# Kernel tuning notes

Measured on AMD Instinct MI355X. Metric: run time of the kernel, lower is better.

Reference implementation:

```python
import jax, jax.numpy as jnp
import numpy as np

B, N, C_IN, C_OUT = 2, 512, 64, 64  # mid_dim == out_dim
EPS = 1e-5

def _bn(x, g, b):
    # PyTorch BatchNorm1d in training mode: biased batch stats over axis 0 of [M, C]
    mu = x.mean(axis=0)
    var = x.var(axis=0)
    return (x - mu) * jax.lax.rsqrt(var + EPS) * g + b

def setup_inputs() -> dict:
    key = jax.random.key(0)
    ks = jax.random.split(key, 16)
    s = 0.05
    return {
        "pos": jax.random.normal(ks[0], (B, N, 3), jnp.float32),
        "c_features": jax.random.normal(ks[1], (B, N, C_IN), jnp.float32),
        "Wq": jax.random.normal(ks[2], (C_OUT, C_IN), jnp.float32) * s,
        "bq": jnp.zeros((C_OUT,), jnp.float32),
        "Wk": jax.random.normal(ks[3], (C_OUT, C_IN), jnp.float32) * s,
        "bk": jnp.zeros((C_OUT,), jnp.float32),
        "Wv": jax.random.normal(ks[4], (C_OUT, C_IN), jnp.float32) * s,
        "bv": jnp.zeros((C_OUT,), jnp.float32),
        "Wp1": jax.random.normal(ks[5], (3, 3), jnp.float32) * s,
        "bp1": jnp.zeros((3,), jnp.float32),
        "g_p": jnp.ones((3,), jnp.float32),
        "b_p": jnp.zeros((3,), jnp.float32),
        "Wp2": jax.random.normal(ks[6], (C_OUT, 3), jnp.float32) * s,
        "bp2": jnp.zeros((C_OUT,), jnp.float32),
        "g_w": jnp.ones((C_OUT,), jnp.float32),
        "b_w": jnp.zeros((C_OUT,), jnp.float32),
        "Ww1": jax.random.normal(ks[7], (C_OUT, C_OUT), jnp.float32) * s,
        "bw1": jnp.zeros((C_OUT,), jnp.float32),
        "Ww2": jax.random.normal(ks[8], (C_OUT, C_OUT), jnp.float32) * s,
        "bw2": jnp.zeros((C_OUT,), jnp.float32),
    }

def reference(pos, c_features, Wq, bq, Wk, bk, Wv, bv, Wp1, bp1, g_p, b_p, Wp2, bp2, g_w, b_w, Ww1, bw1, Ww2, bw2):
    b, n = pos.shape[0], pos.shape[1]
    q = c_features @ Wq.T + bq                       # [B,N,Cmid]
    k = c_features @ Wk.T + bk
    v = c_features @ Wv.T + bv                       # [B,N,Cout]
    rel = pos[:, :, None, :] - pos[:, None, :, :]    # [B,N,N,3]
    h = rel.reshape(-1, 3) @ Wp1.T + bp1             # [B*N*N,3]
    h = jax.nn.relu(_bn(h, g_p, b_p))
    delta = (h @ Wp2.T + bp2).reshape(b, n, n, -1)   # [B,N,N,Cmid]
    qk = q[:, :, None, :] - k[:, None, :, :] + delta # [B,N,N,Cmid]
    h2 = _bn(qk.reshape(-1, qk.shape[-1]), g_w, b_w)
    h2 = jax.nn.relu(h2)
    h2 = jax.nn.relu(h2 @ Ww1.T + bw1)
    w = (h2 @ Ww2.T + bw2).reshape(b, n, n, -1)      # [B,N,N,Cout]
    attn = jax.nn.softmax(w, axis=2)                 # softmax over j
    out = jnp.sum(attn * (v[:, None, :, :] + delta), axis=2)  # [B,N,Cout]
    return out
```

## Files before the change

kernel.cpp:

```cpp
#include <hip/hip_runtime.h>
#include <stdint.h>
#include <stddef.h>

#define DEV __device__ __forceinline__

typedef __attribute__((ext_vector_type(4))) float f32x4;
typedef __attribute__((ext_vector_type(8))) short bf16x8;

union FragU { bf16x8 f; uint32_t u[4]; };

DEV uint32_t pk_bf16(float a, float b) {
  uint32_t d;
  asm("v_cvt_pk_bf16_f32 %0, %1, %2" : "=v"(d) : "v"(a), "v"(b));
  return d;
}

DEV uint16_t f2bf(float x) {
  uint32_t u = __float_as_uint(x);
  u += 0x7fffu + ((u >> 16) & 1u);
  return (uint16_t)(u >> 16);
}

__launch_bounds__(256)
__global__ void kP(const float* __restrict__ cf, const float* __restrict__ pos,
                   const float* __restrict__ Wq, const float* __restrict__ Wk,
                   const float* __restrict__ Wv, const float* __restrict__ bq,
                   const float* __restrict__ bk, const float* __restrict__ bv,
                   const float* __restrict__ Ww1, const float* __restrict__ Ww2,
                   const float* __restrict__ Wp1, const float* __restrict__ g_p,
                   const float* __restrict__ bp2,
                   float* __restrict__ qo, float* __restrict__ ko,
                   float* __restrict__ vT, uint16_t* __restrict__ W1bf,
                   uint16_t* __restrict__ W2bf, float* __restrict__ a1out,
                   unsigned int* __restrict__ counter) {
  const int bid = blockIdx.x, t = threadIdx.x;
  if (bid < 256) {
    __shared__ float cfl[4][64];
    const int rr = t >> 6, c = t & 63;
    const int r0 = bid * 4;
    cfl[rr][c] = cf[(size_t)(r0 + rr) * 64 + c];
    __syncthreads();
    const int bn = r0 + rr;
    const float* wqr = Wq + c * 64;
    const float* wkr = Wk + c * 64;
    const float* wvr = Wv + c * 64;
    float aq = bq[c], ak = bk[c], av = bv[c] + bp2[c];
#pragma unroll 8
    for (int kk = 0; kk < 64; ++kk) {
      const float f = cfl[rr][kk];
      aq = fmaf(f, wqr[kk], aq);
      ak = fmaf(f, wkr[kk], ak);
      av = fmaf(f, wvr[kk], av);
    }
    qo[(size_t)bn * 64 + c] = aq;
    ko[(size_t)bn * 64 + c] = ak;
    vT[((size_t)(bn >> 9) * 64 + c) * 512 + (bn & 511)] = av;
  } else if (bid == 256) {
    for (int idx = t; idx < 8192; idx += 256) {
      const int m = idx >> 12;
      const int r = idx & 4095;
      const int f = r >> 9;
      const int l = (r >> 3) & 63;
      const int e = r & 7;
      const int nt = f >> 1, ks = f & 1, lm = l & 15, lq = l >> 4;
      const int row = 16 * nt + lm, col = 8 * lq + 32 * ks + e;
      const float src = m ? Ww2[row * 64 + col] : Ww1[row * 64 + col];
      (m ? W2bf : W1bf)[r] = f2bf(src);
    }
  } else {
    if (t == 0) counter[0] = 0u;
    __shared__ float acc9[2][9];
    __shared__ float red[256][10];
    __shared__ float red2[9][16];
    for (int b = 0; b < 2; ++b) {
      float s[9];
#pragma unroll
      for (int a = 0; a < 9; ++a) s[a] = 0.f;
      for (int r = 0; r < 2; ++r) {
        int i = t + 256 * r;
        const float* p = pos + (size_t)(b * 512 + i) * 3;
        float p0 = p[0], p1 = p[1], p2 = p[2];
        s[0] += p0; s[1] += p1; s[2] += p2;
        s[3] += p0 * p0; s[4] += p0 * p1; s[5] += p0 * p2;
        s[6] += p1 * p1; s[7] += p1 * p2; s[8] += p2 * p2;
      }
#pragma unroll
      for (int a = 0; a < 9; ++a) red[t][a] = s[a];
      __syncthreads();
      if (t < 144) {
        const int a = t >> 4, p = t & 15;
        float v = 0.f;
#pragma unroll
        for (int qq = 0; qq < 16; ++qq) v += red[p * 16 + qq][a];
        red2[a][p] = v;
      }
      __syncthreads();
      if (t < 9) {
        float v = 0.f;
#pragma unroll
        for (int p = 0; p < 16; ++p) v += red2[t][p];
        acc9[b][t] = v;
      }
      __syncthreads();
    }
    if (t == 0) {
      float C[6] = {0.f, 0.f, 0.f, 0.f, 0.f, 0.f};
      const float invM = 1.0f / 524288.0f;
      for (int b = 0; b < 2; ++b) {
        float S0 = acc9[b][0], S1 = acc9[b][1], S2 = acc9[b][2];
        float G00 = acc9[b][3], G01 = acc9[b][4], G02 = acc9[b][5];
        float G11 = acc9[b][6], G12 = acc9[b][7], G22 = acc9[b][8];
        C[0] += 1024.f * G00 - 2.f * S0 * S0;
        C[1] += 1024.f * G01 - 2.f * S0 * S1;
        C[2] += 1024.f * G02 - 2.f * S0 * S2;
        C[3] += 1024.f * G11 - 2.f * S1 * S1;
        C[4] += 1024.f * G12 - 2.f * S1 * S2;
        C[5] += 1024.f * G22 - 2.f * S2 * S2;
      }
      for (int a = 0; a < 6; ++a) C[a] *= invM;
      for (int tt = 0; tt < 3; ++tt) {
        float w0 = Wp1[tt * 3 + 0], w1 = Wp1[tt * 3 + 1], w2 = Wp1[tt * 3 + 2];
        float var = w0 * w0 * C[0] + w1 * w1 * C[3] + w2 * w2 * C[5]
                  + 2.f * (w0 * w1 * C[1] + w0 * w2 * C[2] + w1 * w2 * C[4]);
        a1out[tt] = g_p[tt] * rsqrtf(var + 1e-5f);
      }
      a1out[3] = 0.f;
    }
  }
}

__launch_bounds__(256)
__global__ void kB(const float* __restrict__ pos, const float* __restrict__ a1,
                   const float* __restrict__ Wp1, const float* __restrict__ b_p,
                   const float* __restrict__ q, const float* __restrict__ k,
                   const float* __restrict__ bp2,
                   const float* __restrict__ g_w, const float* __restrict__ b_w,
                   const float* __restrict__ Wp2,
                   float* __restrict__ hpa, float* __restrict__ Mpart,
                   float* __restrict__ XPp, float* __restrict__ SNp,
                   unsigned int* __restrict__ counter,
                   float* __restrict__ a2o, float* __restrict__ be2o,
                   float* __restrict__ PtT) {
  const int bid = blockIdx.x, t = threadIdx.x;
  const int s = bid >> 4, b = (bid >> 3) & 1, chunk = bid & 7;

  __shared__ __align__(16) f32x4 X[512];
  __shared__ float U[64][64];
  __shared__ float redr[64][4][4];
  __shared__ float mred[256][6];
  __shared__ float mred2[64][6];
  __shared__ float rfin[64][4];
  __shared__ float redn[256][2];
  __shared__ float MfS[6];
  __shared__ float ShfS[3];
  __shared__ unsigned int isLast;

  {
    const float a10 = a1[0], a11 = a1[1], a12 = a1[2];
    const float w00 = Wp1[0], w01 = Wp1[1], w02 = Wp1[2];
    const float w10 = Wp1[3], w11 = Wp1[4], w12 = Wp1[5];
    const float w20 = Wp1[6], w21 = Wp1[7], w22 = Wp1[8];
    for (int r = 0; r < 2; ++r) {
      const int row = t + 256 * r;
      const float* p = pos + (size_t)(b * 512 + row) * 3;
      const float p0 = p[0], p1 = p[1], p2 = p[2];
      f32x4 v;
      v.x = a10 * (w00 * p0 + w01 * p1 + w02 * p2);
      v.y = a11 * (w10 * p0 + w11 * p1 + w12 * p2);
      v.z = a12 * (w20 * p0 + w21 * p1 + w22 * p2);
      v.w = 0.f;
      if (s == 0 && chunk == 0)
        *(f32x4*)(hpa + (size_t)(b * 512 + row) * 4) = v;
      if (s) { v.x = -v.x; v.y = -v.y; v.z = -v.z; }
      X[row] = v;
    }
  }
  {
    const float* src = s ? k : q;
    const int r0g = b * 512 + chunk * 64;
#pragma unroll
    for (int e = 0; e < 16; ++e) {
      const int idx = e * 256 + t;
      const int row = idx >> 6, c = idx & 63;
      float v = src[(size_t)(r0g + row) * 64 + c];
      if (!s) v += bp2[c];
      U[row][c] = v;
    }
  }
  __syncthreads();

  {
    const int al = t >> 2, qr = t & 3;
    const int a = chunk * 64 + al;
    const f32x4 xa = X[a];
    const float base0 = xa.x + b_p[0], base1 = xa.y + b_p[1], base2 = xa.z + b_p[2];
    float r0 = 0, r1 = 0, r2 = 0;
    float m00 = 0, m01 = 0, m02 = 0, m11 = 0, m12 = 0, m22 = 0;
#pragma unroll 8
    for (int jj = qr * 128; jj < qr * 128 + 128; ++jj) {
      const f32x4 xj = X[jj];
      const float h0 = fmaxf(0.f, base0 - xj.x);
      const float h1 = fmaxf(0.f, base1 - xj.y);
      const float h2 = fmaxf(0.f, base2 - xj.z);
      r0 += h0; r1 += h1; r2 += h2;
      if (s == 0) {
        m00 = fmaf(h0, h0, m00); m01 = fmaf(h0, h1, m01); m02 = fmaf(h0, h2, m02);
        m11 = fmaf(h1, h1, m11); m12 = fmaf(h1, h2, m12); m22 = fmaf(h2, h2, m22);
      }
    }
    redr[al][qr][0] = r0; redr[al][qr][1] = r1; redr[al][qr][2] = r2; redr[al][qr][3] = 0.f;
    mred[t][0] = m00; mred[t][1] = m01; mred[t][2] = m02;
    mred[t][3] = m11; mred[t][4] = m12; mred[t][5] = m22;
  }
  __syncthreads();

  if (t < 64) {
    float sx = 0, sy = 0, sz = 0;
#pragma unroll
    for (int p = 0; p < 4; ++p) { sx += redr[t][p][0]; sy += redr[t][p][1]; sz += redr[t][p][2]; }
    rfin[t][0] = sx; rfin[t][1] = sy; rfin[t][2] = sz; rfin[t][3] = 0.f;
    if (s == 0) {
#pragma unroll
      for (int cc = 0; cc < 6; ++cc)
        mred2[t][cc] = mred[t][cc] + mred[t + 64][cc] + mred[t + 128][cc] + mred[t + 192][cc];
    }
  }
  __syncthreads();

  if (s == 0 && t < 6) {
    float m = 0.f;
    for (int p = 0; p < 64; ++p) m += mred2[p][t];
    Mpart[bid * 12 + t] = m;
  }
  if (s == 0 && t >= 64 && t < 67) {
    const int tt = t - 64;
    float v = 0.f;
#pragma unroll 8
    for (int a = 0; a < 64; ++a) v += rfin[a][tt];
    Mpart[bid * 12 + 6 + tt] = v;
  }
  if (t < 192) {
    const int c = t & 63, tt = t >> 6;
    float xp = 0.f;
#pragma unroll 8
    for (int a = 0; a < 64; ++a) xp = fmaf(U[a][c], rfin[a][tt], xp);
    if (s) xp = -xp;
    XPp[((size_t)bid * 3 + tt) * 64 + c] = xp;
  }
  {
    const int c = t & 63, g = t >> 6;
    float su = 0.f, su2 = 0.f;
#pragma unroll
    for (int r = 0; r < 16; ++r) {
      const float v = U[g * 16 + r][c];
      su += v;
      su2 = fmaf(v, v, su2);
    }
    redn[t][0] = su; redn[t][1] = su2;
  }
  __syncthreads();
  if (t < 64) {
    float a0 = 0.f, a1v = 0.f;
#pragma unroll
    for (int p = 0; p < 4; ++p) { a0 += redn[t + 64 * p][0]; a1v += redn[t + 64 * p][1]; }
    SNp[((size_t)bid * 2 + 0) * 64 + t] = a0;
    SNp[((size_t)bid * 2 + 1) * 64 + t] = a1v;
  }

  __syncthreads();
  if (t == 0) {
    __threadfence();
    const unsigned int old = atomicAdd(counter, 1u);
    isLast = (old == 31u) ? 1u : 0u;
  }
  __syncthreads();
  if (isLast) {
    __threadfence();
    if (t < 6) {
      float m = 0.f;
#pragma unroll
      for (int p = 0; p < 16; ++p) m += Mpart[p * 12 + t];
      MfS[t] = m;
    }
    if (t >= 6 && t < 9) {
      const int tt = t - 6;
      float v = 0.f;
#pragma unroll
      for (int p = 0; p < 16; ++p) v += Mpart[p * 12 + 6 + tt];
      ShfS[tt] = v;
    }
    __syncthreads();
    if (t < 64) {
      const int c = t;
      float Su[2], Su2[2], Sk[2], Sk2[2];
#pragma unroll
      for (int bb = 0; bb < 2; ++bb) {
        float a0 = 0.f, a1v = 0.f, a2v = 0.f, a3 = 0.f;
#pragma unroll
        for (int p = 0; p < 8; ++p) {
          const int blkU = bb * 8 + p;
          const int blkK = 16 + bb * 8 + p;
          a0 += SNp[((size_t)blkU * 2 + 0) * 64 + c];
          a1v += SNp[((size_t)blkU * 2 + 1) * 64 + c];
          a2v += SNp[((size_t)blkK * 2 + 0) * 64 + c];
          a3 += SNp[((size_t)blkK * 2 + 1) * 64 + c];
        }
        Su[bb] = a0; Su2[bb] = a1v; Sk[bb] = a2v; Sk2[bb] = a3;
      }
      float URd0 = 0.f, URd1 = 0.f, URd2 = 0.f;
#pragma unroll
      for (int blk = 0; blk < 32; ++blk) {
        URd0 += XPp[((size_t)blk * 3 + 0) * 64 + c];
        URd1 += XPp[((size_t)blk * 3 + 1) * 64 + c];
        URd2 += XPp[((size_t)blk * 3 + 2) * 64 + c];
      }
      const float P0t = Wp2[c * 3 + 0], P1t = Wp2[c * 3 + 1], P2t = Wp2[c * 3 + 2];
      const float Nf = 512.f, invM = 1.f / 524288.f;
      float S1 = 0.f, Q2 = 0.f;
#pragma unroll
      for (int bb = 0; bb < 2; ++bb) {
        S1 += Nf * (Su[bb] - Sk[bb]);
        Q2 += Nf * Su2[bb] - 2.f * Su[bb] * Sk[bb] + Nf * Sk2[bb];
      }
      const float Xc = P0t * URd0 + P1t * URd1 + P2t * URd2;
      S1 += P0t * ShfS[0] + P1t * ShfS[1] + P2t * ShfS[2];
      const float Hm = P0t * P0t * MfS[0] + 2.f * P0t * P1t * MfS[1] + 2.f * P0t * P2t * MfS[2]
                     + P1t * P1t * MfS[3] + 2.f * P1t * P2t * MfS[4] + P2t * P2t * MfS[5];
      const float E1 = S1 * invM;
      const float E2 = (Q2 + 2.f * Xc + Hm) * invM;
      const float var = E2 - E1 * E1;
      const float rstd = rsqrtf(var + 1e-5f);
      const float A2 = g_w[c] * rstd;
      a2o[c] = A2;
      be2o[c] = b_w[c] - E1 * A2;
      PtT[0 * 64 + c] = A2 * P0t;
      PtT[1 * 64 + c] = A2 * P1t;
      PtT[2 * 64 + c] = A2 * P2t;
    }
  }
}

__launch_bounds__(256)
__global__ void k3_main(const float* __restrict__ q, const float* __restrict__ kk_,
                        const float* __restrict__ vT, const float* __restrict__ hpa,
                        const float* __restrict__ a2g, const float* __restrict__ be2g,
                        const float* __restrict__ PtTg,
                        const uint16_t* __restrict__ W1bf, const uint16_t* __restrict__ W2bf,
                        const float* __restrict__ bp2, const float* __restrict__ Wp2,
                        const float* __restrict__ b_p, const float* __restrict__ bw1g,
                        const float* __restrict__ bw2g, float* __restrict__ out) {
  const int bid = blockIdx.x;
  const int b = bid >> 9, i = bid & 511;
  const int t = threadIdx.x;
  const int wid = t >> 6, l = t & 63;
  const int lm = l & 15, lq = l >> 4;

  __shared__ __align__(16) uint16_t W1l[4096];
  __shared__ __align__(16) uint16_t W2l[4096];
  __shared__ __align__(16) uint16_t H2[4][16][76];
  __shared__ __align__(16) float P0[64];
  __shared__ __align__(16) float a2s[64];
  __shared__ __align__(16) float Pts[3][64];
  __shared__ __align__(16) float comb[4][64][2];

  {
    *(bf16x8*)(&W1l[t * 16])     = *(const bf16x8*)(W1bf + t * 16);
    *(bf16x8*)(&W1l[t * 16 + 8]) = *(const bf16x8*)(W1bf + t * 16 + 8);
    *(bf16x8*)(&W2l[t * 16])     = *(const bf16x8*)(W2bf + t * 16);
    *(bf16x8*)(&W2l[t * 16 + 8]) = *(const bf16x8*)(W2bf + t * 16 + 8);
  }
  if (t < 64) {
    const float a2v = a2g[t];
    a2s[t] = a2v;
    P0[t] = fmaf(a2v, q[(size_t)(b * 512 + i) * 64 + t] + bp2[t], be2g[t]);
  } else {
    const int idx = t - 64;
    Pts[idx >> 6][idx & 63] = PtTg[idx];
  }

  const f32x4 hi = *(const f32x4*)(hpa + (size_t)(b * 512 + i) * 4);
  const float bb0 = b_p[0], bb1 = b_p[1], bb2 = b_p[2];
  const float LOG2E = 1.4426950408889634f;

  float bw1r[4], bw2l[4], wpa[4], wpb[4], wpc[4];
#pragma unroll
  for (int nt = 0; nt < 4; ++nt) {
    const int c = 16 * nt + lm;
    bw1r[nt] = bw1g[c];
    bw2l[nt] = bw2g[c] * LOG2E;
    wpa[nt] = Wp2[c * 3 + 0];
    wpb[nt] = Wp2[c * 3 + 1];
    wpc[nt] = Wp2[c * 3 + 2];
  }

  float l_[4] = {0.f, 0.f, 0.f, 0.f};
  float acc_[4] = {0.f, 0.f, 0.f, 0.f};

  __syncthreads();

  const float* kbase = kk_ + (size_t)(b * 512) * 64;
  const float* hbase = hpa + (size_t)(b * 512) * 4;
  const float* vTb = vT + (size_t)b * 64 * 512;

  for (int it = 0; it < 8; ++it) {
    const int jb = it * 64 + wid * 16;
    const int j = jb + lm;
    const int j2 = jb + 4 * lq;

    f32x4 kv[2][2];
#pragma unroll
    for (int ks = 0; ks < 2; ++ks) {
      kv[ks][0] = *(const f32x4*)(kbase + (size_t)j * 64 + 32 * ks + 8 * lq);
      kv[ks][1] = *(const f32x4*)(kbase + (size_t)j * 64 + 32 * ks + 8 * lq + 4);
    }
    const f32x4 hj = *(const f32x4*)(hbase + j * 4);
    f32x4 hjr[4];
#pragma unroll
    for (int r = 0; r < 4; ++r) hjr[r] = *(const f32x4*)(hbase + (j2 + r) * 4);
    f32x4 vv[4];
#pragma unroll
    for (int nt = 0; nt < 4; ++nt)
      vv[nt] = *(const f32x4*)(vTb + (size_t)(16 * nt + lm) * 512 + j2);

    const float h0 = fmaxf(0.f, hi.x - hj.x + bb0);
    const float h1 = fmaxf(0.f, hi.y - hj.y + bb1);
    const float h2v = fmaxf(0.f, hi.z - hj.z + bb2);

    FragU A1[2];
#pragma unroll
    for (int ks = 0; ks < 2; ++ks) {
      const int c0 = 32 * ks + 8 * lq;
      f32x4 pv[2], av[2], t0[2], t1[2], t2[2];
      pv[0] = *(const f32x4*)(P0 + c0);        pv[1] = *(const f32x4*)(P0 + c0 + 4);
      av[0] = *(const f32x4*)(a2s + c0);       av[1] = *(const f32x4*)(a2s + c0 + 4);
      t0[0] = *(const f32x4*)(&Pts[0][c0]);    t0[1] = *(const f32x4*)(&Pts[0][c0 + 4]);
      t1[0] = *(const f32x4*)(&Pts[1][c0]);    t1[1] = *(const f32x4*)(&Pts[1][c0 + 4]);
      t2[0] = *(const f32x4*)(&Pts[2][c0]);    t2[1] = *(const f32x4*)(&Pts[2][c0 + 4]);
      float x[8];
#pragma unroll
      for (int e = 0; e < 8; ++e) {
        const int hh = e >> 2, e4 = e & 3;
        float xv = pv[hh][e4] - av[hh][e4] * kv[ks][hh][e4];
        xv = fmaf(t0[hh][e4], h0, xv);
        xv = fmaf(t1[hh][e4], h1, xv);
        xv = fmaf(t2[hh][e4], h2v, xv);
        x[e] = fmaxf(0.f, xv);
      }
      A1[ks].u[0] = pk_bf16(x[0], x[1]);
      A1[ks].u[1] = pk_bf16(x[2], x[3]);
      A1[ks].u[2] = pk_bf16(x[4], x[5]);
      A1[ks].u[3] = pk_bf16(x[6], x[7]);
    }

    f32x4 d1[4];
#pragma unroll
    for (int nt = 0; nt < 4; ++nt) {
      FragU b0, b1;
      b0.f = *(const bf16x8*)(&W1l[((nt * 2 + 0) * 64 + l) * 8]);
      b1.f = *(const bf16x8*)(&W1l[((nt * 2 + 1) * 64 + l) * 8]);
      f32x4 z = {0.f, 0.f, 0.f, 0.f};
      z = __builtin_amdgcn_mfma_f32_16x16x32_bf16(A1[0].f, b0.f, z, 0, 0, 0);
      z = __builtin_amdgcn_mfma_f32_16x16x32_bf16(A1[1].f, b1.f, z, 0, 0, 0);
      d1[nt] = z;
    }

    uint16_t (*h2w)[76] = H2[wid];
#pragma unroll
    for (int nt = 0; nt < 4; ++nt) {
      const float e0 = fmaxf(0.f, d1[nt][0] + bw1r[nt]);
      const float e1 = fmaxf(0.f, d1[nt][1] + bw1r[nt]);
      const float e2 = fmaxf(0.f, d1[nt][2] + bw1r[nt]);
      const float e3 = fmaxf(0.f, d1[nt][3] + bw1r[nt]);
      const uint32_t u01 = pk_bf16(e0, e1);
      const uint32_t u23 = pk_bf16(e2, e3);
      const int col = 16 * nt + lm;
      h2w[4 * lq + 0][col] = (uint16_t)(u01 & 0xffffu);
      h2w[4 * lq + 1][col] = (uint16_t)(u01 >> 16);
      h2w[4 * lq + 2][col] = (uint16_t)(u23 & 0xffffu);
      h2w[4 * lq + 3][col] = (uint16_t)(u23 >> 16);
    }

    FragU A2[2];
    A2[0].f = *(const bf16x8*)(&h2w[lm][8 * lq]);
    A2[1].f = *(const bf16x8*)(&h2w[lm][32 + 8 * lq]);

    f32x4 d2[4];
#pragma unroll
    for (int nt = 0; nt < 4; ++nt) {
      FragU b0, b1;
      b0.f = *(const bf16x8*)(&W2l[((nt * 2 + 0) * 64 + l) * 8]);
      b1.f = *(const bf16x8*)(&W2l[((nt * 2 + 1) * 64 + l) * 8]);
      f32x4 z = {0.f, 0.f, 0.f, 0.f};
      z = __builtin_amdgcn_mfma_f32_16x16x32_bf16(A2[0].f, b0.f, z, 0, 0, 0);
      z = __builtin_amdgcn_mfma_f32_16x16x32_bf16(A2[1].f, b1.f, z, 0, 0, 0);
      d2[nt] = z;
    }

    float hr0[4], hr1[4], hr2[4];
#pragma unroll
    for (int r = 0; r < 4; ++r) {
      hr0[r] = fmaxf(0.f, hi.x - hjr[r].x + bb0);
      hr1[r] = fmaxf(0.f, hi.y - hjr[r].y + bb1);
      hr2[r] = fmaxf(0.f, hi.z - hjr[r].z + bb2);
    }

#pragma unroll
    for (int nt = 0; nt < 4; ++nt) {
      float p[4], val[4];
#pragma unroll
      for (int r = 0; r < 4; ++r) {
        p[r] = __builtin_amdgcn_exp2f(fmaf(d2[nt][r], LOG2E, bw2l[nt]));
        float v0 = vv[nt][r];
        v0 = fmaf(wpa[nt], hr0[r], v0);
        v0 = fmaf(wpb[nt], hr1[r], v0);
        v0 = fmaf(wpc[nt], hr2[r], v0);
        val[r] = v0;
      }
      l_[nt] += (p[0] + p[1]) + (p[2] + p[3]);
      float a = acc_[nt];
      a = fmaf(p[0], val[0], a);
      a = fmaf(p[1], val[1], a);
      a = fmaf(p[2], val[2], a);
      a = fmaf(p[3], val[3], a);
      acc_[nt] = a;
    }
  }

#pragma unroll
  for (int nt = 0; nt < 4; ++nt) {
    l_[nt] += __shfl_xor(l_[nt], 16);
    acc_[nt] += __shfl_xor(acc_[nt], 16);
    l_[nt] += __shfl_xor(l_[nt], 32);
    acc_[nt] += __shfl_xor(acc_[nt], 32);
  }
  if (lq == 0) {
#pragma unroll
    for (int nt = 0; nt < 4; ++nt) {
      comb[wid][16 * nt + lm][0] = l_[nt];
      comb[wid][16 * nt + lm][1] = acc_[nt];
    }
  }
  __syncthreads();
  if (t < 64) {
    float L = 0.f, A = 0.f;
#pragma unroll
    for (int w = 0; w < 4; ++w) {
      L += comb[w][t][0];
      A += comb[w][t][1];
    }
    out[(size_t)(b * 512 + i) * 64 + t] = A / L;
  }
}

extern "C" void kernel_launch(void* const* d_in, const int* in_sizes, int n_in,
                              void* d_out, int out_size, void* d_ws, size_t ws_size,
                              hipStream_t stream) {
  (void)in_sizes; (void)n_in; (void)out_size; (void)ws_size;
  const float* pos = (const float*)d_in[0];
  const float* cf  = (const float*)d_in[1];
  const float* Wq  = (const float*)d_in[2];
  const float* bq  = (const float*)d_in[3];
  const float* Wk  = (const float*)d_in[4];
  const float* bk  = (const float*)d_in[5];
  const float* Wv  = (const float*)d_in[6];
  const float* bv  = (const float*)d_in[7];
  const float* Wp1 = (const float*)d_in[8];
  const float* g_p = (const float*)d_in[10];
  const float* b_p = (const float*)d_in[11];
  const float* Wp2 = (const float*)d_in[12];
  const float* bp2 = (const float*)d_in[13];
  const float* g_w = (const float*)d_in[14];
  const float* b_w = (const float*)d_in[15];
  const float* Ww1 = (const float*)d_in[16];
  const float* bw1 = (const float*)d_in[17];
  const float* Ww2 = (const float*)d_in[18];
  const float* bw2 = (const float*)d_in[19];

  char* ws = (char*)d_ws;
  uint16_t*     W1bf = (uint16_t*)(ws + 0);
  uint16_t*     W2bf = (uint16_t*)(ws + 8192);
  float*        a1w  = (float*)(ws + 16384);
  unsigned int* cnt  = (unsigned int*)(ws + 16640);
  float*        hpaw = (float*)(ws + 16896);
  float*        qw   = (float*)(ws + 33280);
  float*        kw   = (float*)(ws + 295424);
  float*        vTw  = (float*)(ws + 557568);
  float*        Mpw  = (float*)(ws + 819712);
  float*        XPpw = (float*)(ws + 821248);
  float*        SNpw = (float*)(ws + 845824);
  float*        a2w  = (float*)(ws + 862208);
  float*        be2w = (float*)(ws + 862464);
  float*        PtTw = (float*)(ws + 862720);

  kP<<<dim3(258), dim3(256), 0, stream>>>(cf, pos, Wq, Wk, Wv, bq, bk, bv,
                                          Ww1, Ww2, Wp1, g_p, bp2,
                                          qw, kw, vTw, W1bf, W2bf, a1w, cnt);
  kB<<<dim3(32), dim3(256), 0, stream>>>(pos, a1w, Wp1, b_p, qw, kw, bp2,
                                         g_w, b_w, Wp2,
                                         hpaw, Mpw, XPpw, SNpw, cnt,
                                         a2w, be2w, PtTw);
  k3_main<<<dim3(1024), dim3(256), 0, stream>>>(qw, kw, vTw, hpaw, a2w, be2w, PtTw,
                                                W1bf, W2bf, bp2, Wp2, b_p, bw1, bw2,
                                                (float*)d_out);
}
```

Baseline: 72.43 us.

## Process two query rows per block over half the keys, add combine kernel

Each k3_main block now handles two query rows i and half of the j range. The loaded k, v and pos data and the W1 fragments are reused across both rows, and a new small kernel k4 sums the two halves' softmax partials and divides. W2 is pre-scaled by log2(e) and read directly from global instead of LDS, both biases are folded into the MFMA accumulator init, and launch bounds request 4 blocks per CU. The partial buffer reuses workspace memory overlapping the BN scratch, and the extra kernel launch plus the doubled register pressure per thread are the costs.

```diff
diff --git a/kernel.cpp b/kernel.cpp
--- a/kernel.cpp
+++ b/kernel.cpp
@@ -56,6 +56,7 @@
     ko[(size_t)bn * 64 + c] = ak;
     vT[((size_t)(bn >> 9) * 64 + c) * 512 + (bn & 511)] = av;
   } else if (bid == 256) {
+    const float L2E = 1.4426950408889634f;
     for (int idx = t; idx < 8192; idx += 256) {
       const int m = idx >> 12;
       const int r = idx & 4095;
@@ -64,7 +65,7 @@
       const int e = r & 7;
       const int nt = f >> 1, ks = f & 1, lm = l & 15, lq = l >> 4;
       const int row = 16 * nt + lm, col = 8 * lq + 32 * ks + e;
-      const float src = m ? Ww2[row * 64 + col] : Ww1[row * 64 + col];
+      const float src = m ? (Ww2[row * 64 + col] * L2E) : Ww1[row * 64 + col];
       (m ? W2bf : W1bf)[r] = f2bf(src);
     }
   } else {
@@ -340,7 +341,7 @@
   }
 }
 
-__launch_bounds__(256)
+__launch_bounds__(256, 4)
 __global__ void k3_main(const float* __restrict__ q, const float* __restrict__ kk_,
                         const float* __restrict__ vT, const float* __restrict__ hpa,
                         const float* __restrict__ a2g, const float* __restrict__ be2g,
@@ -348,37 +349,39 @@
                         const uint16_t* __restrict__ W1bf, const uint16_t* __restrict__ W2bf,
                         const float* __restrict__ bp2, const float* __restrict__ Wp2,
                         const float* __restrict__ b_p, const float* __restrict__ bw1g,
-                        const float* __restrict__ bw2g, float* __restrict__ out) {
+                        const float* __restrict__ bw2g, float* __restrict__ Pout) {
   const int bid = blockIdx.x;
-  const int b = bid >> 9, i = bid & 511;
+  const int b = bid >> 9, rem = bid & 511;
+  const int ipair = rem >> 1, half = rem & 1;
+  const int i0 = ipair * 2;
   const int t = threadIdx.x;
   const int wid = t >> 6, l = t & 63;
   const int lm = l & 15, lq = l >> 4;
 
   __shared__ __align__(16) uint16_t W1l[4096];
-  __shared__ __align__(16) uint16_t W2l[4096];
-  __shared__ __align__(16) uint16_t H2[4][16][76];
-  __shared__ __align__(16) float P0[64];
+  __shared__ __align__(16) uint16_t H2[4][2][16][76];
+  __shared__ __align__(16) float P0L[2][64];
   __shared__ __align__(16) float a2s[64];
   __shared__ __align__(16) float Pts[3][64];
-  __shared__ __align__(16) float comb[4][64][2];
-
-  {
-    *(bf16x8*)(&W1l[t * 16])     = *(const bf16x8*)(W1bf + t * 16);
-    *(bf16x8*)(&W1l[t * 16 + 8]) = *(const bf16x8*)(W1bf + t * 16 + 8);
-    *(bf16x8*)(&W2l[t * 16])     = *(const bf16x8*)(W2bf + t * 16);
-    *(bf16x8*)(&W2l[t * 16 + 8]) = *(const bf16x8*)(W2bf + t * 16 + 8);
-  }
-  if (t < 64) {
-    const float a2v = a2g[t];
-    a2s[t] = a2v;
-    P0[t] = fmaf(a2v, q[(size_t)(b * 512 + i) * 64 + t] + bp2[t], be2g[t]);
+  __shared__ __align__(16) float comb[4][2][64][2];
+
+  *(bf16x8*)(&W1l[t * 16])     = *(const bf16x8*)(W1bf + t * 16);
+  *(bf16x8*)(&W1l[t * 16 + 8]) = *(const bf16x8*)(W1bf + t * 16 + 8);
+  if (t < 128) {
+    const int ii = t >> 6, c = t & 63;
+    P0L[ii][c] = fmaf(a2g[c], q[(size_t)(b * 512 + i0 + ii) * 64 + c] + bp2[c], be2g[c]);
+  } else if (t < 192) {
+    const int c = t - 128;
+    a2s[c] = a2g[c];
   } else {
-    const int idx = t - 64;
-    Pts[idx >> 6][idx & 63] = PtTg[idx];
-  }
-
-  const f32x4 hi = *(const f32x4*)(hpa + (size_t)(b * 512 + i) * 4);
+    const int c = t - 192;
+    Pts[0][c] = PtTg[c];
+    Pts[1][c] = PtTg[64 + c];
+    Pts[2][c] = PtTg[128 + c];
+  }
+
+  const f32x4 hi0 = *(const f32x4*)(hpa + (size_t)(b * 512 + i0) * 4);
+  const f32x4 hi1 = *(const f32x4*)(hpa + (size_t)(b * 512 + i0 + 1) * 4);
   const float bb0 = b_p[0], bb1 = b_p[1], bb2 = b_p[2];
   const float LOG2E = 1.4426950408889634f;
 
@@ -393,8 +396,8 @@
     wpc[nt] = Wp2[c * 3 + 2];
   }
 
-  float l_[4] = {0.f, 0.f, 0.f, 0.f};
-  float acc_[4] = {0.f, 0.f, 0.f, 0.f};
+  float l0_[4] = {0.f, 0.f, 0.f, 0.f}, a0_[4] = {0.f, 0.f, 0.f, 0.f};
+  float l1_[4] = {0.f, 0.f, 0.f, 0.f}, a1_[4] = {0.f, 0.f, 0.f, 0.f};
 
   __syncthreads();
 
@@ -402,8 +405,8 @@
   const float* hbase = hpa + (size_t)(b * 512) * 4;
   const float* vTb = vT + (size_t)b * 64 * 512;
 
-  for (int it = 0; it < 8; ++it) {
-    const int jb = it * 64 + wid * 16;
+  for (int it = 0; it < 4; ++it) {
+    const int jb = half * 256 + it * 64 + wid * 16;
     const int j = jb + lm;
     const int j2 = jb + 4 * lq;
 
@@ -414,142 +417,206 @@
       kv[ks][1] = *(const f32x4*)(kbase + (size_t)j * 64 + 32 * ks + 8 * lq + 4);
     }
     const f32x4 hj = *(const f32x4*)(hbase + j * 4);
-    f32x4 hjr[4];
-#pragma unroll
-    for (int r = 0; r < 4; ++r) hjr[r] = *(const f32x4*)(hbase + (j2 + r) * 4);
+
+    const float h00 = fmaxf(0.f, hi0.x - hj.x + bb0);
+    const float h01 = fmaxf(0.f, hi0.y - hj.y + bb1);
+    const float h02 = fmaxf(0.f, hi0.z - hj.z + bb2);
+    const float h10 = fmaxf(0.f, hi1.x - hj.x + bb0);
+    const float h11 = fmaxf(0.f, hi1.y - hj.y + bb1);
+    const float h12 = fmaxf(0.f, hi1.z - hj.z + bb2);
+
+    FragU A1a[2], A1b[2];
+#pragma unroll
+    for (int ks = 0; ks < 2; ++ks) {
+      float x0[8], x1[8];
+#pragma unroll
+      for (int hh = 0; hh < 2; ++hh) {
+        const int c0 = 32 * ks + 8 * lq + 4 * hh;
+        const f32x4 av = *(const f32x4*)(a2s + c0);
+        const f32x4 t0v = *(const f32x4*)(&Pts[0][c0]);
+        const f32x4 t1v = *(const f32x4*)(&Pts[1][c0]);
+        const f32x4 t2v = *(const f32x4*)(&Pts[2][c0]);
+        const f32x4 p0v = *(const f32x4*)(&P0L[0][c0]);
+        const f32x4 p1v = *(const f32x4*)(&P0L[1][c0]);
+#pragma unroll
+        for (int e = 0; e < 4; ++e) {
+          const float nak = -av[e] * kv[ks][hh][e];
+          float xv0 = p0v[e] + nak;
+          xv0 = fmaf(t0v[e], h00, xv0);
+          xv0 = fmaf(t1v[e], h01, xv0);
+          xv0 = fmaf(t2v[e], h02, xv0);
+          x0[4 * hh + e] = fmaxf(0.f, xv0);
+          float xv1 = p1v[e] + nak;
+          xv1 = fmaf(t0v[e], h10, xv1);
+          xv1 = fmaf(t1v[e], h11, xv1);
+          xv1 = fmaf(t2v[e], h12, xv1);
+          x1[4 * hh + e] = fmaxf(0.f, xv1);
+        }
+      }
+      A1a[ks].u[0] = pk_bf16(x0[0], x0[1]);
+      A1a[ks].u[1] = pk_bf16(x0[2], x0[3]);
+      A1a[ks].u[2] = pk_bf16(x0[4], x0[5]);
+      A1a[ks].u[3] = pk_bf16(x0[6], x0[7]);
+      A1b[ks].u[0] = pk_bf16(x1[0], x1[1]);
+      A1b[ks].u[1] = pk_bf16(x1[2], x1[3]);
+      A1b[ks].u[2] = pk_bf16(x1[4], x1[5]);
+      A1b[ks].u[3] = pk_bf16(x1[6], x1[7]);
+    }
+
+    f32x4 d1a[4], d1b[4];
+#pragma unroll
+    for (int nt = 0; nt < 4; ++nt) {
+      FragU w0, w1;
+      w0.f = *(const bf16x8*)(&W1l[((nt * 2 + 0) * 64 + l) * 8]);
+      w1.f = *(const bf16x8*)(&W1l[((nt * 2 + 1) * 64 + l) * 8]);
+      f32x4 z0 = {bw1r[nt], bw1r[nt], bw1r[nt], bw1r[nt]};
+      z0 = __builtin_amdgcn_mfma_f32_16x16x32_bf16(A1a[0].f, w0.f, z0, 0, 0, 0);
+      z0 = __builtin_amdgcn_mfma_f32_16x16x32_bf16(A1a[1].f, w1.f, z0, 0, 0, 0);
+      d1a[nt] = z0;
+      f32x4 z1 = {bw1r[nt], bw1r[nt], bw1r[nt], bw1r[nt]};
+      z1 = __builtin_amdgcn_mfma_f32_16x16x32_bf16(A1b[0].f, w0.f, z1, 0, 0, 0);
+      z1 = __builtin_amdgcn_mfma_f32_16x16x32_bf16(A1b[1].f, w1.f, z1, 0, 0, 0);
+      d1b[nt] = z1;
+    }
+
+    {
+      uint16_t (*h2w)[76] = H2[wid][0];
+#pragma unroll
+      for (int nt = 0; nt < 4; ++nt) {
+        const uint32_t u01 = pk_bf16(fmaxf(0.f, d1a[nt][0]), fmaxf(0.f, d1a[nt][1]));
+        const uint32_t u23 = pk_bf16(fmaxf(0.f, d1a[nt][2]), fmaxf(0.f, d1a[nt][3]));
+        const int col = 16 * nt + lm;
+        h2w[4 * lq + 0][col] = (uint16_t)(u01 & 0xffffu);
+        h2w[4 * lq + 1][col] = (uint16_t)(u01 >> 16);
+        h2w[4 * lq + 2][col] = (uint16_t)(u23 & 0xffffu);
+        h2w[4 * lq + 3][col] = (uint16_t)(u23 >> 16);
+      }
+    }
+    {
+      uint16_t (*h2w)[76] = H2[wid][1];
+#pragma unroll
+      for (int nt = 0; nt < 4; ++nt) {
+        const uint32_t u01 = pk_bf16(fmaxf(0.f, d1b[nt][0]), fmaxf(0.f, d1b[nt][1]));
+        const uint32_t u23 = pk_bf16(fmaxf(0.f, d1b[nt][2]), fmaxf(0.f, d1b[nt][3]));
+        const int col = 16 * nt + lm;
+        h2w[4 * lq + 0][col] = (uint16_t)(u01 & 0xffffu);
+        h2w[4 * lq + 1][col] = (uint16_t)(u01 >> 16);
+        h2w[4 * lq + 2][col] = (uint16_t)(u23 & 0xffffu);
+        h2w[4 * lq + 3][col] = (uint16_t)(u23 >> 16);
+      }
+    }
+
+    FragU A2a[2], A2b[2];
+    A2a[0].f = *(const bf16x8*)(&H2[wid][0][lm][8 * lq]);
+    A2a[1].f = *(const bf16x8*)(&H2[wid][0][lm][32 + 8 * lq]);
+    A2b[0].f = *(const bf16x8*)(&H2[wid][1][lm][8 * lq]);
+    A2b[1].f = *(const bf16x8*)(&H2[wid][1][lm][32 + 8 * lq]);
+
+    f32x4 d2a[4], d2b[4];
+#pragma unroll
+    for (int nt = 0; nt < 4; ++nt) {
+      FragU w0, w1;
+      w0.f = *(const bf16x8*)(W2bf + ((nt * 2 + 0) * 64 + l) * 8);
+      w1.f = *(const bf16x8*)(W2bf + ((nt * 2 + 1) * 64 + l) * 8);
+      f32x4 z0 = {bw2l[nt], bw2l[nt], bw2l[nt], bw2l[nt]};
+      z0 = __builtin_amdgcn_mfma_f32_16x16x32_bf16(A2a[0].f, w0.f, z0, 0, 0, 0);
+      z0 = __builtin_amdgcn_mfma_f32_16x16x32_bf16(A2a[1].f, w1.f, z0, 0, 0, 0);
+      d2a[nt] = z0;
+      f32x4 z1 = {bw2l[nt], bw2l[nt], bw2l[nt], bw2l[nt]};
+      z1 = __builtin_amdgcn_mfma_f32_16x16x32_bf16(A2b[0].f, w0.f, z1, 0, 0, 0);
+      z1 = __builtin_amdgcn_mfma_f32_16x16x32_bf16(A2b[1].f, w1.f, z1, 0, 0, 0);
+      d2b[nt] = z1;
+    }
+
     f32x4 vv[4];
 #pragma unroll
     for (int nt = 0; nt < 4; ++nt)
       vv[nt] = *(const f32x4*)(vTb + (size_t)(16 * nt + lm) * 512 + j2);
-
-    const float h0 = fmaxf(0.f, hi.x - hj.x + bb0);
-    const float h1 = fmaxf(0.f, hi.y - hj.y + bb1);
-    const float h2v = fmaxf(0.f, hi.z - hj.z + bb2);
-
-    FragU A1[2];
-#pragma unroll
-    for (int ks = 0; ks < 2; ++ks) {
-      const int c0 = 32 * ks + 8 * lq;
-      f32x4 pv[2], av[2], t0[2], t1[2], t2[2];
-      pv[0] = *(const f32x4*)(P0 + c0);        pv[1] = *(const f32x4*)(P0 + c0 + 4);
-      av[0] = *(const f32x4*)(a2s + c0);       av[1] = *(const f32x4*)(a2s + c0 + 4);
-      t0[0] = *(const f32x4*)(&Pts[0][c0]);    t0[1] = *(const f32x4*)(&Pts[0][c0 + 4]);
-      t1[0] = *(const f32x4*)(&Pts[1][c0]);    t1[1] = *(const f32x4*)(&Pts[1][c0 + 4]);
-      t2[0] = *(const f32x4*)(&Pts[2][c0]);    t2[1] = *(const f32x4*)(&Pts[2][c0 + 4]);
-      float x[8];
-#pragma unroll
-      for (int e = 0; e < 8; ++e) {
-        const int hh = e >> 2, e4 = e & 3;
-        float xv = pv[hh][e4] - av[hh][e4] * kv[ks][hh][e4];
-        xv = fmaf(t0[hh][e4], h0, xv);
-        xv = fmaf(t1[hh][e4], h1, xv);
-        xv = fmaf(t2[hh][e4], h2v, xv);
-        x[e] = fmaxf(0.f, xv);
-      }
-      A1[ks].u[0] = pk_bf16(x[0], x[1]);
-      A1[ks].u[1] = pk_bf16(x[2], x[3]);
-      A1[ks].u[2] = pk_bf16(x[4], x[5]);
-      A1[ks].u[3] = pk_bf16(x[6], x[7]);
-    }
-
-    f32x4 d1[4];
+    f32x4 hjr[4];
+#pragma unroll
+    for (int r = 0; r < 4; ++r) hjr[r] = *(const f32x4*)(hbase + (j2 + r) * 4);
+
+    float hr00[4], hr01[4], hr02[4], hr10[4], hr11[4], hr12[4];
+#pragma unroll
+    for (int r = 0; r < 4; ++r) {
+      hr00[r] = fmaxf(0.f, hi0.x - hjr[r].x + bb0);
+      hr01[r] = fmaxf(0.f, hi0.y - hjr[r].y + bb1);
+      hr02[r] = fmaxf(0.f, hi0.z - hjr[r].z + bb2);
+      hr10[r] = fmaxf(0.f, hi1.x - hjr[r].x + bb0);
+      hr11[r] = fmaxf(0.f, hi1.y - hjr[r].y + bb1);
+      hr12[r] = fmaxf(0.f, hi1.z - hjr[r].z + bb2);
+    }
+
 #pragma unroll
     for (int nt = 0; nt < 4; ++nt) {
-      FragU b0, b1;
-      b0.f = *(const bf16x8*)(&W1l[((nt * 2 + 0) * 64 + l) * 8]);
-      b1.f = *(const bf16x8*)(&W1l[((nt * 2 + 1) * 64 + l) * 8]);
-      f32x4 z = {0.f, 0.f, 0.f, 0.f};
-      z = __builtin_amdgcn_mfma_f32_16x16x32_bf16(A1[0].f, b0.f, z, 0, 0, 0);
-      z = __builtin_amdgcn_mfma_f32_16x16x32_bf16(A1[1].f, b1.f, z, 0, 0, 0);
-      d1[nt] = z;
-    }
-
-    uint16_t (*h2w)[76] = H2[wid];
+      float p0[4], p1[4], va[4], vb[4];
+#pragma unroll
+      for (int r = 0; r < 4; ++r) {
+        p0[r] = __builtin_amdgcn_exp2f(d2a[nt][r]);
+        p1[r] = __builtin_amdgcn_exp2f(d2b[nt][r]);
+        const float vvr = vv[nt][r];
+        float v0 = fmaf(wpa[nt], hr00[r], vvr);
+        v0 = fmaf(wpb[nt], hr01[r], v0);
+        v0 = fmaf(wpc[nt], hr02[r], v0);
+        va[r] = v0;
+        float v1 = fmaf(wpa[nt], hr10[r], vvr);
+        v1 = fmaf(wpb[nt], hr11[r], v1);
+        v1 = fmaf(wpc[nt], hr12[r], v1);
+        vb[r] = v1;
+      }
+      l0_[nt] += (p0[0] + p0[1]) + (p0[2] + p0[3]);
+      l1_[nt] += (p1[0] + p1[1]) + (p1[2] + p1[3]);
+      float aa = a0_[nt];
+      aa = fmaf(p0[0], va[0], aa); aa = fmaf(p0[1], va[1], aa);
+      aa = fmaf(p0[2], va[2], aa); aa = fmaf(p0[3], va[3], aa);
+      a0_[nt] = aa;
+      float ab = a1_[nt];
+      ab = fmaf(p1[0], vb[0], ab); ab = fmaf(p1[1], vb[1], ab);
+      ab = fmaf(p1[2], vb[2], ab); ab = fmaf(p1[3], vb[3], ab);
+      a1_[nt] = ab;
+    }
+  }
+
+#pragma unroll
+  for (int nt = 0; nt < 4; ++nt) {
+    l0_[nt] += __shfl_xor(l0_[nt], 16); a0_[nt] += __shfl_xor(a0_[nt], 16);
+    l0_[nt] += __shfl_xor(l0_[nt], 32); a0_[nt] += __shfl_xor(a0_[nt], 32);
+    l1_[nt] += __shfl_xor(l1_[nt], 16); a1_[nt] += __shfl_xor(a1_[nt], 16);
+    l1_[nt] += __shfl_xor(l1_[nt], 32); a1_[nt] += __shfl_xor(a1_[nt], 32);
+  }
+  if (lq == 0) {
 #pragma unroll
     for (int nt = 0; nt < 4; ++nt) {
-      const float e0 = fmaxf(0.f, d1[nt][0] + bw1r[nt]);
-      const float e1 = fmaxf(0.f, d1[nt][1] + bw1r[nt]);
-      const float e2 = fmaxf(0.f, d1[nt][2] + bw1r[nt]);
-      const float e3 = fmaxf(0.f, d1[nt][3] + bw1r[nt]);
-      const uint32_t u01 = pk_bf16(e0, e1);
-      const uint32_t u23 = pk_bf16(e2, e3);
-      const int col = 16 * nt + lm;
-      h2w[4 * lq + 0][col] = (uint16_t)(u01 & 0xffffu);
-      h2w[4 * lq + 1][col] = (uint16_t)(u01 >> 16);
-      h2w[4 * lq + 2][col] = (uint16_t)(u23 & 0xffffu);
-      h2w[4 * lq + 3][col] = (uint16_t)(u23 >> 16);
-    }
-
-    FragU A2[2];
-    A2[0].f = *(const bf16x8*)(&h2w[lm][8 * lq]);
-    A2[1].f = *(const bf16x8*)(&h2w[lm][32 + 8 * lq]);
-
-    f32x4 d2[4];
-#pragma unroll
-    for (int nt = 0; nt < 4; ++nt) {
-      FragU b0, b1;
-      b0.f = *(const bf16x8*)(&W2l[((nt * 2 + 0) * 64 + l) * 8]);
-      b1.f = *(const bf16x8*)(&W2l[((nt * 2 + 1) * 64 + l) * 8]);
-      f32x4 z = {0.f, 0.f, 0.f, 0.f};
-      z = __builtin_amdgcn_mfma_f32_16x16x32_bf16(A2[0].f, b0.f, z, 0, 0, 0);
-      z = __builtin_amdgcn_mfma_f32_16x16x32_bf16(A2[1].f, b1.f, z, 0, 0, 0);
-      d2[nt] = z;
-    }
-
-    float hr0[4], hr1[4], hr2[4];
-#pragma unroll
-    for (int r = 0; r < 4; ++r) {
-      hr0[r] = fmaxf(0.f, hi.x - hjr[r].x + bb0);
-      hr1[r] = fmaxf(0.f, hi.y - hjr[r].y + bb1);
-      hr2[r] = fmaxf(0.f, hi.z - hjr[r].z + bb2);
-    }
-
-#pragma unroll
-    for (int nt = 0; nt < 4; ++nt) {
-      float p[4], val[4];
-#pragma unroll
-      for (int r = 0; r < 4; ++r) {
-        p[r] = __builtin_amdgcn_exp2f(fmaf(d2[nt][r], LOG2E, bw2l[nt]));
-        float v0 = vv[nt][r];
-        v0 = fmaf(wpa[nt], hr0[r], v0);
-        v0 = fmaf(wpb[nt], hr1[r], v0);
-        v0 = fmaf(wpc[nt], hr2[r], v0);
-        val[r] = v0;
-      }
-      l_[nt] += (p[0] + p[1]) + (p[2] + p[3]);
-      float a = acc_[nt];
-      a = fmaf(p[0], val[0], a);
-      a = fmaf(p[1], val[1], a);
-      a = fmaf(p[2], val[2], a);
-      a = fmaf(p[3], val[3], a);
-      acc_[nt] = a;
-    }
-  }
-
-#pragma unroll
-  for (int nt = 0; nt < 4; ++nt) {
-    l_[nt] += __shfl_xor(l_[nt], 16);
-    acc_[nt] += __shfl_xor(acc_[nt], 16);
-    l_[nt] += __shfl_xor(l_[nt], 32);
-    acc_[nt] += __shfl_xor(acc_[nt], 32);
-  }
-  if (lq == 0) {
-#pragma unroll
-    for (int nt = 0; nt < 4; ++nt) {
-      comb[wid][16 * nt + lm][0] = l_[nt];
-      comb[wid][16 * nt + lm][1] = acc_[nt];
-    }
-  }
-  __syncthreads();
-  if (t < 64) {
+      comb[wid][0][16 * nt + lm][0] = l0_[nt];
+      comb[wid][0][16 * nt + lm][1] = a0_[nt];
+      comb[wid][1][16 * nt + lm][0] = l1_[nt];
+      comb[wid][1][16 * nt + lm][1] = a1_[nt];
+    }
+  }
+  __syncthreads();
+  if (t < 128) {
+    const int ii = t >> 6, c = t & 63;
     float L = 0.f, A = 0.f;
 #pragma unroll
     for (int w = 0; w < 4; ++w) {
-      L += comb[w][t][0];
-      A += comb[w][t][1];
-    }
-    out[(size_t)(b * 512 + i) * 64 + t] = A / L;
-  }
+      L += comb[w][ii][c][0];
+      A += comb[w][ii][c][1];
+    }
+    Pout[(size_t)bid * 256 + ii * 128 + c] = L;
+    Pout[(size_t)bid * 256 + ii * 128 + 64 + c] = A;
+  }
+}
+
+__launch_bounds__(256)
+__global__ void k4(const float* __restrict__ Pout, float* __restrict__ out) {
+  const int g = blockIdx.x * 256 + threadIdx.x;
+  const int row = g >> 6, c = g & 63;
+  const int b = row >> 9, i = row & 511;
+  const int ipair = i >> 1, sub = i & 1;
+  const size_t base = (size_t)((b << 9) | (ipair << 1)) * 256 + sub * 128 + c;
+  const float L = Pout[base] + Pout[base + 256];
+  const float A = Pout[base + 64] + Pout[base + 320];
+  out[(size_t)row * 64 + c] = A / L;
 }
 
 extern "C" void kernel_launch(void* const* d_in, const int* in_sizes, int n_in,
@@ -585,12 +652,13 @@
   float*        qw   = (float*)(ws + 33280);
   float*        kw   = (float*)(ws + 295424);
   float*        vTw  = (float*)(ws + 557568);
-  float*        Mpw  = (float*)(ws + 819712);
-  float*        XPpw = (float*)(ws + 821248);
-  float*        SNpw = (float*)(ws + 845824);
-  float*        a2w  = (float*)(ws + 862208);
-  float*        be2w = (float*)(ws + 862464);
-  float*        PtTw = (float*)(ws + 862720);
+  float*        a2w  = (float*)(ws + 819712);
+  float*        be2w = (float*)(ws + 819968);
+  float*        PtTw = (float*)(ws + 820224);
+  float*        Mpw  = (float*)(ws + 821248);
+  float*        XPpw = (float*)(ws + 823040);
+  float*        SNpw = (float*)(ws + 847872);
+  float*        Pow  = (float*)(ws + 821248);
 
   kP<<<dim3(258), dim3(256), 0, stream>>>(cf, pos, Wq, Wk, Wv, bq, bk, bv,
                                           Ww1, Ww2, Wp1, g_p, bp2,
@@ -601,5 +669,6 @@
                                          a2w, be2w, PtTw);
   k3_main<<<dim3(1024), dim3(256), 0, stream>>>(qw, kw, vTw, hpaw, a2w, be2w, PtTw,
                                                 W1bf, W2bf, bp2, Wp2, b_p, bw1, bw2,
-                                                (float*)d_out);
+                                                Pow);
+  k4<<<dim3(256), dim3(256), 0, stream>>>(Pow, (float*)d_out);
 }
```

Result: slower. 133.0 us (+83.6%).
